# Kernel optimization log

Measured on AMD Instinct MI355X. Metric: run time of the kernel, lower is better.

## Reference

```python
import jax, jax.numpy as jnp
import numpy as np

B, F = 8192, 256  # batch, nfeat


def setup_inputs() -> dict:
    key = jax.random.key(0)
    ks = jax.random.split(key, 6)
    return {
        "x": jax.random.normal(ks[0], (B, F), dtype=jnp.float32),
        "W1": jax.random.normal(ks[1], (F, 100), dtype=jnp.float32) * 0.1,  # fc1 weight (in=1)
        "b1": jax.random.normal(ks[2], (F, 100), dtype=jnp.float32) * 0.1,
        "W2": jax.random.normal(ks[3], (F, 50, 100), dtype=jnp.float32) * 0.1,  # fc2 [out,in] per feature
        "b2": jax.random.normal(ks[4], (F, 50), dtype=jnp.float32) * 0.1,
        "W3": jax.random.normal(ks[5], (F, 50), dtype=jnp.float32) * 0.1,  # fc3, no bias
        "bias": jnp.zeros((1,), dtype=jnp.float32),  # NAM global _bias
    }


def reference(x, W1, b1, W2, b2, W3, bias):
    # fc1: per-feature Linear(1,100) -> outer product along feature dim
    h1 = jax.nn.relu(x[:, :, None] * W1[None, :, :] + b1[None, :, :])  # [B,F,100]
    # fc2: per-feature Linear(100,50) as batched GEMM over feature dim
    h2 = jax.nn.relu(jnp.einsum("bfh,foh->bfo", h1, W2) + b2[None, :, :])  # [B,F,50]
    # fc3: per-feature Linear(50,1, bias=False) -> per-feature scalar contribution
    f = jnp.einsum("bfo,fo->bf", h2, W3)  # [B,F]
    # sum over features + global bias, sigmoid
    return jax.nn.sigmoid(f.sum(axis=-1) + bias[0])  # [B]
```

## Files before the change

### kernel.cpp

```cpp
#include <hip/hip_runtime.h>
#include <math.h>

#define BATCH 8192
#define NFEAT 256
#define NH1   100
#define NH2   50
#define KP    128
#define FPB   8
#define RPB   256

typedef __attribute__((ext_vector_type(8))) _Float16 half8;
typedef __attribute__((ext_vector_type(2))) _Float16 h2v;
typedef __attribute__((ext_vector_type(4))) float    float4v;

#define OFF_W1H  (NFEAT * 8192 / 2)
#define OFF_B1H  (OFF_W1H + NFEAT * KP / 2)

__global__ __launch_bounds__(256) void prep(
    const float* __restrict__ W1, const float* __restrict__ b1,
    const float* __restrict__ W2, float* __restrict__ ws,
    float* __restrict__ out)
{
    __shared__ float l2[NH2 * 40];
    const int q = blockIdx.x;
    const int f = blockIdx.y;
    const int t = threadIdx.x;

    if (q == 0) {
        _Float16* w1h = (_Float16*)(ws + OFF_W1H) + f * KP;
        _Float16* b1h = (_Float16*)(ws + OFF_B1H) + f * KP;
        if (t < KP) {
            w1h[t] = (_Float16)((t < NH1) ? W1[f * NH1 + t] : 0.f);
            b1h[t] = (_Float16)((t < NH1) ? b1[f * NH1 + t] : 0.f);
        }
        if (t < 32) out[f * 32 + t] = 0.f;
    }

    const float* __restrict__ w2g = W2 + (size_t)f * NH2 * NH1;
#pragma unroll
    for (int i = 0; i < 7; ++i) {
        const int idx = i * 256 + t;
        if (idx < NH2 * 32) {
            const int o = idx >> 5, hh = idx & 31, h = q * 32 + hh;
            l2[o * 40 + hh] = (h < NH1) ? w2g[o * NH1 + h] : 0.f;
        }
    }
    __syncthreads();

    _Float16* w2h = (_Float16*)ws + (size_t)f * 8192 + q * 2048;
#pragma unroll
    for (int i = 0; i < 8; ++i) {
        const int el   = i * 256 + t;
        const int j    = el & 7;
        const int lane = (el >> 3) & 63;
        const int nt   = (el >> 9) & 3;
        const int o    = nt * 16 + (lane & 15);
        const int hl   = (lane >> 4) * 8 + j;
        w2h[el] = (_Float16)((o < NH2) ? l2[o * 40 + hl] : 0.f);
    }
}

__device__ __forceinline__ void stage_async(
    const _Float16* __restrict__ src, _Float16* dst, int t)
{
#pragma unroll
    for (int i = 0; i < 2; ++i) {
        const _Float16* g = src + (i * 512 + t) * 8;
        _Float16* l       = dst + (i * 512 + t) * 8;
        __builtin_amdgcn_global_load_lds(
            (const __attribute__((address_space(1))) unsigned*)g,
            (__attribute__((address_space(3))) unsigned*)l, 16, 0, 0);
    }
}

__global__ __launch_bounds__(512, 4) void nam_mfma(
    const float* __restrict__ x,
    const float* __restrict__ ws,
    const float* __restrict__ b2,
    const float* __restrict__ W3,
    float* __restrict__ out)
{
    __shared__ _Float16 lds[2][8192];
    __shared__ _Float16 xshh[FPB * RPB];
    __shared__ _Float16 wsh[FPB * KP];
    __shared__ _Float16 csh[FPB * KP];

    const int t   = threadIdx.x;
    const int wv  = t >> 6;
    const int l64 = t & 63;
    const int ln  = t & 15;
    const int qd  = (t >> 4) & 3;
    const int rowbase = blockIdx.x * RPB + wv * 32;
    const int f0      = blockIdx.y * FPB;

    const _Float16* w2h = (const _Float16*)ws;
    const _Float16* w1h = (const _Float16*)(ws + OFF_W1H);
    const _Float16* b1h = (const _Float16*)(ws + OFF_B1H);

    int osrc[4];
#pragma unroll
    for (int nt = 0; nt < 4; ++nt) {
        const int o = nt * 16 + ln;
        osrc[nt] = (o < NH2) ? o : 0;
    }

    stage_async(w2h + (size_t)f0 * 8192, lds[0], t);
    {
        const int r = t >> 1, half = t & 1;
        const float4 v = *(const float4*)(
            x + (size_t)(blockIdx.x * RPB + r) * NFEAT + f0 + half * 4);
        xshh[(half * 4 + 0) * RPB + r] = (_Float16)v.x;
        xshh[(half * 4 + 1) * RPB + r] = (_Float16)v.y;
        xshh[(half * 4 + 2) * RPB + r] = (_Float16)v.z;
        xshh[(half * 4 + 3) * RPB + r] = (_Float16)v.w;
    }
    if (t < 128)
        ((int4*)wsh)[t] = ((const int4*)(w1h + (size_t)f0 * KP))[t];
    else if (t < 256)
        ((int4*)csh)[t - 128] = ((const int4*)(b1h + (size_t)f0 * KP))[t - 128];
    __syncthreads();

    float rp[2][4] = {{0.f}, {0.f}};

#pragma unroll 1
    for (int fi = 0; fi < FPB; ++fi) {
        const int f = f0 + fi;
        const _Float16* B = lds[fi & 1];

        if (fi + 1 < FPB)
            stage_async(w2h + (size_t)(f + 1) * 8192, lds[(fi + 1) & 1], t);

        h2v xh[2];
#pragma unroll
        for (int mt = 0; mt < 2; ++mt) {
            const _Float16 xs = xshh[fi * RPB + wv * 32 + mt * 16 + ln];
            xh[mt] = (h2v){xs, xs};
        }

        float4v acc[2][4];
#pragma unroll
        for (int mt = 0; mt < 2; ++mt)
#pragma unroll
            for (int nt = 0; nt < 4; ++nt) acc[mt][nt] = (float4v){0.f, 0.f, 0.f, 0.f};

        const h2v z2 = (h2v){(_Float16)0.f, (_Float16)0.f};

#pragma unroll
        for (int kk = 0; kk < 4; ++kk) {
            half8 bf[4];
#pragma unroll
            for (int nt = 0; nt < 4; ++nt)
                bf[nt] = *(const half8*)(B + (kk * 4 + nt) * 512 + l64 * 8);

            const half8 wv8 = *(const half8*)(wsh + fi * KP + kk * 32 + qd * 8);
            const half8 cv8 = *(const half8*)(csh + fi * KP + kk * 32 + qd * 8);
            const h2v* wpp = (const h2v*)&wv8;
            const h2v* cpp = (const h2v*)&cv8;

#pragma unroll
            for (int mt = 0; mt < 2; ++mt) {
                half8 af;
                h2v* ap = (h2v*)&af;
                ap[0] = __builtin_elementwise_max(wpp[0] * xh[mt] + cpp[0], z2);
                ap[1] = __builtin_elementwise_max(wpp[1] * xh[mt] + cpp[1], z2);
                ap[2] = __builtin_elementwise_max(wpp[2] * xh[mt] + cpp[2], z2);
                ap[3] = __builtin_elementwise_max(wpp[3] * xh[mt] + cpp[3], z2);
#pragma unroll
                for (int nt = 0; nt < 4; ++nt)
                    acc[mt][nt] = __builtin_amdgcn_mfma_f32_16x16x32_f16(
                        af, bf[nt], acc[mt][nt], 0, 0, 0);
            }
        }

        const float* __restrict__ b2g = b2 + f * NH2;
        const float* __restrict__ w3g = W3 + f * NH2;
#pragma unroll
        for (int nt = 0; nt < 4; ++nt) {
            const int o = nt * 16 + ln;
            const float bo = b2g[osrc[nt]];
            const float wo = (o < NH2) ? w3g[osrc[nt]] : 0.f;
#pragma unroll
            for (int mt = 0; mt < 2; ++mt)
#pragma unroll
                for (int r = 0; r < 4; ++r)
                    rp[mt][r] = fmaf(fmaxf(acc[mt][nt][r] + bo, 0.f), wo, rp[mt][r]);
        }

        __syncthreads();
    }

#pragma unroll
    for (int mt = 0; mt < 2; ++mt)
#pragma unroll
        for (int r = 0; r < 4; ++r) {
            float v = rp[mt][r];
            v += __shfl_xor(v, 1);
            v += __shfl_xor(v, 2);
            v += __shfl_xor(v, 4);
            v += __shfl_xor(v, 8);
            if (ln == 0)
                atomicAdd(out + rowbase + mt * 16 + qd * 4 + r, v);
        }
}

__global__ __launch_bounds__(256) void nam_finish(
    float* __restrict__ out, const float* __restrict__ bias)
{
    const int b = blockIdx.x * blockDim.x + threadIdx.x;
    out[b] = 1.0f / (1.0f + expf(-(out[b] + bias[0])));
}

extern "C" void kernel_launch(void* const* d_in, const int* in_sizes, int n_in,
                              void* d_out, int out_size, void* d_ws, size_t ws_size,
                              hipStream_t stream) {
    const float* x    = (const float*)d_in[0];
    const float* W1   = (const float*)d_in[1];
    const float* b1   = (const float*)d_in[2];
    const float* W2   = (const float*)d_in[3];
    const float* b2   = (const float*)d_in[4];
    const float* W3   = (const float*)d_in[5];
    const float* bias = (const float*)d_in[6];
    float* out = (float*)d_out;
    float* ws  = (float*)d_ws;

    prep<<<dim3(4, NFEAT), 256, 0, stream>>>(W1, b1, W2, ws, out);

    nam_mfma<<<dim3(BATCH / RPB, NFEAT / FPB), 512, 0, stream>>>(
        x, ws, b2, W3, out);

    nam_finish<<<BATCH / 256, 256, 0, stream>>>(out, bias);
}
```

Baseline: 114.2 us.

## Read W2 fragments directly from global memory instead of LDS double buffering

Removes the async global-to-LDS double-buffered staging of the per-feature W2 tiles and has each wave load its B fragments straight from global memory (L2/L1-cached, shared across waves). This drops 32KB of LDS and the per-iteration block barrier, which may raise occupancy and remove sync stalls. The b2 bias is now folded into the accumulator initialisation, and the b2/W3 loads are hoisted to the top of the loop. The cost is that all 8 waves issue redundant global loads for the same tile, with latency no longer hidden by prefetch.

```diff
diff --git a/kernel.cpp b/kernel.cpp
--- a/kernel.cpp
+++ b/kernel.cpp
@@ -60,19 +60,6 @@
     }
 }
 
-__device__ __forceinline__ void stage_async(
-    const _Float16* __restrict__ src, _Float16* dst, int t)
-{
-#pragma unroll
-    for (int i = 0; i < 2; ++i) {
-        const _Float16* g = src + (i * 512 + t) * 8;
-        _Float16* l       = dst + (i * 512 + t) * 8;
-        __builtin_amdgcn_global_load_lds(
-            (const __attribute__((address_space(1))) unsigned*)g,
-            (__attribute__((address_space(3))) unsigned*)l, 16, 0, 0);
-    }
-}
-
 __global__ __launch_bounds__(512, 4) void nam_mfma(
     const float* __restrict__ x,
     const float* __restrict__ ws,
@@ -80,7 +67,6 @@
     const float* __restrict__ W3,
     float* __restrict__ out)
 {
-    __shared__ _Float16 lds[2][8192];
     __shared__ _Float16 xshh[FPB * RPB];
     __shared__ _Float16 wsh[FPB * KP];
     __shared__ _Float16 csh[FPB * KP];
@@ -104,7 +90,6 @@
         osrc[nt] = (o < NH2) ? o : 0;
     }
 
-    stage_async(w2h + (size_t)f0 * 8192, lds[0], t);
     {
         const int r = t >> 1, half = t & 1;
         const float4 v = *(const float4*)(
@@ -122,13 +107,21 @@
 
     float rp[2][4] = {{0.f}, {0.f}};
 
+    const _Float16* __restrict__ Bf = w2h + (size_t)f0 * 8192;
+
 #pragma unroll 1
-    for (int fi = 0; fi < FPB; ++fi) {
+    for (int fi = 0; fi < FPB; ++fi, Bf += 8192) {
         const int f = f0 + fi;
-        const _Float16* B = lds[fi & 1];
-
-        if (fi + 1 < FPB)
-            stage_async(w2h + (size_t)(f + 1) * 8192, lds[(fi + 1) & 1], t);
+
+        const float* __restrict__ b2g = b2 + f * NH2;
+        const float* __restrict__ w3g = W3 + f * NH2;
+        float bo[4], wo[4];
+#pragma unroll
+        for (int nt = 0; nt < 4; ++nt) {
+            const int o = nt * 16 + ln;
+            bo[nt] = b2g[osrc[nt]];
+            wo[nt] = (o < NH2) ? w3g[osrc[nt]] : 0.f;
+        }
 
         h2v xh[2];
 #pragma unroll
@@ -141,7 +134,8 @@
 #pragma unroll
         for (int mt = 0; mt < 2; ++mt)
 #pragma unroll
-            for (int nt = 0; nt < 4; ++nt) acc[mt][nt] = (float4v){0.f, 0.f, 0.f, 0.f};
+            for (int nt = 0; nt < 4; ++nt)
+                acc[mt][nt] = (float4v){bo[nt], bo[nt], bo[nt], bo[nt]};
 
         const h2v z2 = (h2v){(_Float16)0.f, (_Float16)0.f};
 
@@ -150,7 +144,7 @@
             half8 bf[4];
 #pragma unroll
             for (int nt = 0; nt < 4; ++nt)
-                bf[nt] = *(const half8*)(B + (kk * 4 + nt) * 512 + l64 * 8);
+                bf[nt] = *(const half8*)(Bf + (kk * 4 + nt) * 512 + l64 * 8);
 
             const half8 wv8 = *(const half8*)(wsh + fi * KP + kk * 32 + qd * 8);
             const half8 cv8 = *(const half8*)(csh + fi * KP + kk * 32 + qd * 8);
@@ -172,21 +166,13 @@
             }
         }
 
-        const float* __restrict__ b2g = b2 + f * NH2;
-        const float* __restrict__ w3g = W3 + f * NH2;
-#pragma unroll
-        for (int nt = 0; nt < 4; ++nt) {
-            const int o = nt * 16 + ln;
-            const float bo = b2g[osrc[nt]];
-            const float wo = (o < NH2) ? w3g[osrc[nt]] : 0.f;
+#pragma unroll
+        for (int nt = 0; nt < 4; ++nt)
 #pragma unroll
             for (int mt = 0; mt < 2; ++mt)
 #pragma unroll
                 for (int r = 0; r < 4; ++r)
-                    rp[mt][r] = fmaf(fmaxf(acc[mt][nt][r] + bo, 0.f), wo, rp[mt][r]);
-        }
-
-        __syncthreads();
+                    rp[mt][r] = fmaf(fmaxf(acc[mt][nt][r], 0.f), wo[nt], rp[mt][r]);
     }
 
 #pragma unroll
```

After: 121.9 us. +6.7%, slower.

## Halve block to 4 waves, each computing 64 rows; seed accumulators with b2

Applied to the files above, without the earlier changes.

The block shrinks from 8 to 4 waves. Each wave now handles four 16-row M tiles instead of two, so every B fragment loaded from LDS feeds twice as many MFMAs. Staging loops and x loads are adjusted for 256 threads. The b2 bias is loaded before the GEMM and used as the initial accumulator value, which removes an add from the epilogue. The cost is higher register pressure from the doubled accumulators and fewer waves per block for hiding latency.

```diff
diff --git a/kernel.cpp b/kernel.cpp
--- a/kernel.cpp
+++ b/kernel.cpp
@@ -8,6 +8,7 @@
 #define KP    128
 #define FPB   8
 #define RPB   256
+#define MT    4
 
 typedef __attribute__((ext_vector_type(8))) _Float16 half8;
 typedef __attribute__((ext_vector_type(2))) _Float16 h2v;
@@ -64,16 +65,16 @@
     const _Float16* __restrict__ src, _Float16* dst, int t)
 {
 #pragma unroll
-    for (int i = 0; i < 2; ++i) {
-        const _Float16* g = src + (i * 512 + t) * 8;
-        _Float16* l       = dst + (i * 512 + t) * 8;
+    for (int i = 0; i < 4; ++i) {
+        const _Float16* g = src + (i * 256 + t) * 8;
+        _Float16* l       = dst + (i * 256 + t) * 8;
         __builtin_amdgcn_global_load_lds(
             (const __attribute__((address_space(1))) unsigned*)g,
             (__attribute__((address_space(3))) unsigned*)l, 16, 0, 0);
     }
 }
 
-__global__ __launch_bounds__(512, 4) void nam_mfma(
+__global__ __launch_bounds__(256, 4) void nam_mfma(
     const float* __restrict__ x,
     const float* __restrict__ ws,
     const float* __restrict__ b2,
@@ -90,7 +91,7 @@
     const int l64 = t & 63;
     const int ln  = t & 15;
     const int qd  = (t >> 4) & 3;
-    const int rowbase = blockIdx.x * RPB + wv * 32;
+    const int rowbase = blockIdx.x * RPB + wv * 64;
     const int f0      = blockIdx.y * FPB;
 
     const _Float16* w2h = (const _Float16*)ws;
@@ -105,8 +106,9 @@
     }
 
     stage_async(w2h + (size_t)f0 * 8192, lds[0], t);
-    {
-        const int r = t >> 1, half = t & 1;
+#pragma unroll
+    for (int rr = 0; rr < 2; ++rr) {
+        const int r = rr * 128 + (t >> 1), half = t & 1;
         const float4 v = *(const float4*)(
             x + (size_t)(blockIdx.x * RPB + r) * NFEAT + f0 + half * 4);
         xshh[(half * 4 + 0) * RPB + r] = (_Float16)v.x;
@@ -116,11 +118,11 @@
     }
     if (t < 128)
         ((int4*)wsh)[t] = ((const int4*)(w1h + (size_t)f0 * KP))[t];
-    else if (t < 256)
+    else
         ((int4*)csh)[t - 128] = ((const int4*)(b1h + (size_t)f0 * KP))[t - 128];
     __syncthreads();
 
-    float rp[2][4] = {{0.f}, {0.f}};
+    float rp[MT][4] = {{0.f}, {0.f}, {0.f}, {0.f}};
 
 #pragma unroll 1
     for (int fi = 0; fi < FPB; ++fi) {
@@ -130,18 +132,29 @@
         if (fi + 1 < FPB)
             stage_async(w2h + (size_t)(f + 1) * 8192, lds[(fi + 1) & 1], t);
 
-        h2v xh[2];
-#pragma unroll
-        for (int mt = 0; mt < 2; ++mt) {
-            const _Float16 xs = xshh[fi * RPB + wv * 32 + mt * 16 + ln];
+        const float* __restrict__ b2g = b2 + f * NH2;
+        const float* __restrict__ w3g = W3 + f * NH2;
+        float bo[4], wo[4];
+#pragma unroll
+        for (int nt = 0; nt < 4; ++nt) {
+            const int o = nt * 16 + ln;
+            bo[nt] = b2g[osrc[nt]];
+            wo[nt] = (o < NH2) ? w3g[osrc[nt]] : 0.f;
+        }
+
+        h2v xh[MT];
+#pragma unroll
+        for (int mt = 0; mt < MT; ++mt) {
+            const _Float16 xs = xshh[fi * RPB + wv * 64 + mt * 16 + ln];
             xh[mt] = (h2v){xs, xs};
         }
 
-        float4v acc[2][4];
-#pragma unroll
-        for (int mt = 0; mt < 2; ++mt)
-#pragma unroll
-            for (int nt = 0; nt < 4; ++nt) acc[mt][nt] = (float4v){0.f, 0.f, 0.f, 0.f};
+        float4v acc[MT][4];
+#pragma unroll
+        for (int mt = 0; mt < MT; ++mt)
+#pragma unroll
+            for (int nt = 0; nt < 4; ++nt)
+                acc[mt][nt] = (float4v){bo[nt], bo[nt], bo[nt], bo[nt]};
 
         const h2v z2 = (h2v){(_Float16)0.f, (_Float16)0.f};
 
@@ -158,7 +171,7 @@
             const h2v* cpp = (const h2v*)&cv8;
 
 #pragma unroll
-            for (int mt = 0; mt < 2; ++mt) {
+            for (int mt = 0; mt < MT; ++mt) {
                 half8 af;
                 h2v* ap = (h2v*)&af;
                 ap[0] = __builtin_elementwise_max(wpp[0] * xh[mt] + cpp[0], z2);
@@ -172,25 +185,19 @@
             }
         }
 
-        const float* __restrict__ b2g = b2 + f * NH2;
-        const float* __restrict__ w3g = W3 + f * NH2;
-#pragma unroll
-        for (int nt = 0; nt < 4; ++nt) {
-            const int o = nt * 16 + ln;
-            const float bo = b2g[osrc[nt]];
-            const float wo = (o < NH2) ? w3g[osrc[nt]] : 0.f;
-#pragma unroll
-            for (int mt = 0; mt < 2; ++mt)
+#pragma unroll
+        for (int nt = 0; nt < 4; ++nt)
+#pragma unroll
+            for (int mt = 0; mt < MT; ++mt)
 #pragma unroll
                 for (int r = 0; r < 4; ++r)
-                    rp[mt][r] = fmaf(fmaxf(acc[mt][nt][r] + bo, 0.f), wo, rp[mt][r]);
-        }
+                    rp[mt][r] = fmaf(fmaxf(acc[mt][nt][r], 0.f), wo[nt], rp[mt][r]);
 
         __syncthreads();
     }
 
 #pragma unroll
-    for (int mt = 0; mt < 2; ++mt)
+    for (int mt = 0; mt < MT; ++mt)
 #pragma unroll
         for (int r = 0; r < 4; ++r) {
             float v = rp[mt][r];
@@ -225,7 +232,7 @@
 
     prep<<<dim3(4, NFEAT), 256, 0, stream>>>(W1, b1, W2, ws, out);
 
-    nam_mfma<<<dim3(BATCH / RPB, NFEAT / FPB), 512, 0, stream>>>(
+    nam_mfma<<<dim3(BATCH / RPB, NFEAT / FPB), 256, 0, stream>>>(
         x, ws, b2, W3, out);
 
     nam_finish<<<BATCH / 256, 256, 0, stream>>>(out, bias);
```

Measured after the change: 144.1 us. 26.2% more time.

## Fuse sigmoid finish into MFMA kernel via ticket counter, restructure prep

Applied to the files above, without the earlier changes.

Removes the separate finish kernel launch. The last block per row tile, found with an atomic ticket counter in workspace, applies bias and sigmoid. The prep kernel now uses one 512-thread block per feature that stages all of W2 in LDS and writes half2 pairs. The b2 bias is folded into the accumulator initialisation, and the b2/W3 loads are hoisted before the MFMA loop. The cost is an extra fence and atomic per block, plus reliance on correct memory ordering for the atomically accumulated outputs.

```diff
diff --git a/kernel.cpp b/kernel.cpp
--- a/kernel.cpp
+++ b/kernel.cpp
@@ -15,48 +15,52 @@
 
 #define OFF_W1H  (NFEAT * 8192 / 2)
 #define OFF_B1H  (OFF_W1H + NFEAT * KP / 2)
-
-__global__ __launch_bounds__(256) void prep(
+#define OFF_TKT  (OFF_B1H + NFEAT * KP / 2)
+
+__global__ __launch_bounds__(512) void prep(
     const float* __restrict__ W1, const float* __restrict__ b1,
     const float* __restrict__ W2, float* __restrict__ ws,
     float* __restrict__ out)
 {
-    __shared__ float l2[NH2 * 40];
-    const int q = blockIdx.x;
-    const int f = blockIdx.y;
+    __shared__ float l2[NH2 * 104];
+    const int f = blockIdx.x;
     const int t = threadIdx.x;
 
-    if (q == 0) {
+    if (t < KP) {
         _Float16* w1h = (_Float16*)(ws + OFF_W1H) + f * KP;
+        w1h[t] = (_Float16)((t < NH1) ? W1[f * NH1 + t] : 0.f);
+    } else if (t < 2 * KP) {
         _Float16* b1h = (_Float16*)(ws + OFF_B1H) + f * KP;
-        if (t < KP) {
-            w1h[t] = (_Float16)((t < NH1) ? W1[f * NH1 + t] : 0.f);
-            b1h[t] = (_Float16)((t < NH1) ? b1[f * NH1 + t] : 0.f);
-        }
-        if (t < 32) out[f * 32 + t] = 0.f;
+        const int k = t - KP;
+        b1h[k] = (_Float16)((k < NH1) ? b1[f * NH1 + k] : 0.f);
+    } else if (t < 2 * KP + 32) {
+        out[f * 32 + (t - 2 * KP)] = 0.f;
+    } else if (t == 2 * KP + 32 && f < 32) {
+        ((unsigned*)(ws + OFF_TKT))[f] = 0u;
     }
 
     const float* __restrict__ w2g = W2 + (size_t)f * NH2 * NH1;
-#pragma unroll
-    for (int i = 0; i < 7; ++i) {
-        const int idx = i * 256 + t;
-        if (idx < NH2 * 32) {
-            const int o = idx >> 5, hh = idx & 31, h = q * 32 + hh;
-            l2[o * 40 + hh] = (h < NH1) ? w2g[o * NH1 + h] : 0.f;
-        }
-    }
-    __syncthreads();
-
-    _Float16* w2h = (_Float16*)ws + (size_t)f * 8192 + q * 2048;
+    for (int idx = t; idx < NH2 * NH1; idx += 512)
+        l2[(idx / NH1) * 104 + (idx % NH1)] = w2g[idx];
+    __syncthreads();
+
+    h2v* dst = (h2v*)((_Float16*)ws + (size_t)f * 8192);
 #pragma unroll
     for (int i = 0; i < 8; ++i) {
-        const int el   = i * 256 + t;
+        const int p    = i * 512 + t;
+        const int el   = p * 2;
+        const int q    = el >> 11;
+        const int nt   = (el >> 9) & 3;
+        const int lane = (el >> 3) & 63;
         const int j    = el & 7;
-        const int lane = (el >> 3) & 63;
-        const int nt   = (el >> 9) & 3;
         const int o    = nt * 16 + (lane & 15);
-        const int hl   = (lane >> 4) * 8 + j;
-        w2h[el] = (_Float16)((o < NH2) ? l2[o * 40 + hl] : 0.f);
+        const int h    = q * 32 + ((lane >> 4) << 3) + j;
+        float v0 = 0.f, v1 = 0.f;
+        if (o < NH2) {
+            v0 = (h     < NH1) ? l2[o * 104 + h]     : 0.f;
+            v1 = (h + 1 < NH1) ? l2[o * 104 + h + 1] : 0.f;
+        }
+        dst[p] = (h2v){(_Float16)v0, (_Float16)v1};
     }
 }
 
@@ -78,12 +82,14 @@
     const float* __restrict__ ws,
     const float* __restrict__ b2,
     const float* __restrict__ W3,
+    const float* __restrict__ bias,
     float* __restrict__ out)
 {
     __shared__ _Float16 lds[2][8192];
     __shared__ _Float16 xshh[FPB * RPB];
     __shared__ _Float16 wsh[FPB * KP];
     __shared__ _Float16 csh[FPB * KP];
+    __shared__ unsigned last_flag;
 
     const int t   = threadIdx.x;
     const int wv  = t >> 6;
@@ -130,6 +136,16 @@
         if (fi + 1 < FPB)
             stage_async(w2h + (size_t)(f + 1) * 8192, lds[(fi + 1) & 1], t);
 
+        const float* __restrict__ b2g = b2 + f * NH2;
+        const float* __restrict__ w3g = W3 + f * NH2;
+        float bo[4], wo[4];
+#pragma unroll
+        for (int nt = 0; nt < 4; ++nt) {
+            const int o = nt * 16 + ln;
+            bo[nt] = b2g[osrc[nt]];
+            wo[nt] = (o < NH2) ? w3g[osrc[nt]] : 0.f;
+        }
+
         h2v xh[2];
 #pragma unroll
         for (int mt = 0; mt < 2; ++mt) {
@@ -141,7 +157,8 @@
 #pragma unroll
         for (int mt = 0; mt < 2; ++mt)
 #pragma unroll
-            for (int nt = 0; nt < 4; ++nt) acc[mt][nt] = (float4v){0.f, 0.f, 0.f, 0.f};
+            for (int nt = 0; nt < 4; ++nt)
+                acc[mt][nt] = (float4v){bo[nt], bo[nt], bo[nt], bo[nt]};
 
         const h2v z2 = (h2v){(_Float16)0.f, (_Float16)0.f};
 
@@ -172,19 +189,13 @@
             }
         }
 
-        const float* __restrict__ b2g = b2 + f * NH2;
-        const float* __restrict__ w3g = W3 + f * NH2;
-#pragma unroll
-        for (int nt = 0; nt < 4; ++nt) {
-            const int o = nt * 16 + ln;
-            const float bo = b2g[osrc[nt]];
-            const float wo = (o < NH2) ? w3g[osrc[nt]] : 0.f;
+#pragma unroll
+        for (int nt = 0; nt < 4; ++nt)
 #pragma unroll
             for (int mt = 0; mt < 2; ++mt)
 #pragma unroll
                 for (int r = 0; r < 4; ++r)
-                    rp[mt][r] = fmaf(fmaxf(acc[mt][nt][r] + bo, 0.f), wo, rp[mt][r]);
-        }
+                    rp[mt][r] = fmaf(fmaxf(acc[mt][nt][r], 0.f), wo[nt], rp[mt][r]);
 
         __syncthreads();
     }
@@ -201,13 +212,23 @@
             if (ln == 0)
                 atomicAdd(out + rowbase + mt * 16 + qd * 4 + r, v);
         }
-}
-
-__global__ __launch_bounds__(256) void nam_finish(
-    float* __restrict__ out, const float* __restrict__ bias)
-{
-    const int b = blockIdx.x * blockDim.x + threadIdx.x;
-    out[b] = 1.0f / (1.0f + expf(-(out[b] + bias[0])));
+
+    __syncthreads();
+    if (t == 0) {
+        __threadfence();
+        unsigned* tkt = (unsigned*)(ws + OFF_TKT);
+        const unsigned prev = atomicAdd(tkt + blockIdx.x, 1u);
+        last_flag = (prev == (NFEAT / FPB - 1)) ? 1u : 0u;
+    }
+    __syncthreads();
+    if (last_flag) {
+        __threadfence();
+        if (t < RPB) {
+            const int row = blockIdx.x * RPB + t;
+            const float v = out[row] + bias[0];
+            out[row] = 1.0f / (1.0f + expf(-v));
+        }
+    }
 }
 
 extern "C" void kernel_launch(void* const* d_in, const int* in_sizes, int n_in,
@@ -223,10 +244,8 @@
     float* out = (float*)d_out;
     float* ws  = (float*)d_ws;
 
-    prep<<<dim3(4, NFEAT), 256, 0, stream>>>(W1, b1, W2, ws, out);
+    prep<<<NFEAT, 512, 0, stream>>>(W1, b1, W2, ws, out);
 
     nam_mfma<<<dim3(BATCH / RPB, NFEAT / FPB), 512, 0, stream>>>(
-        x, ws, b2, W3, out);
-
-    nam_finish<<<BATCH / 256, 256, 0, stream>>>(out, bias);
-}
+        x, ws, b2, W3, bias, out);
+}
```

New measurement: 132.2 us. 15.7% more time.
